# Kernel tuning notes

Hardware: AMD Instinct MI355X
Metric: run time of the kernel (lower is better)

Reference implementation:

```python
import jax, jax.numpy as jnp
import numpy as np

H, MEL, ATT, TXT = 1024, 80, 640, 640   # n_hidden, n_mel, n_attn_channels, n_text+n_speaker
T, TTXT = 600, 128


def setup_inputs() -> dict:
    key = jax.random.key(0)
    ks = jax.random.split(key, 20)
    def w(k, shape, s=0.02):
        return (jax.random.normal(k, shape) * s).astype(jnp.float32)
    return {
        "residual": jax.random.normal(ks[0], (T, 1, MEL), jnp.float32),
        "text": jax.random.normal(ks[1], (TTXT, 1, TXT), jnp.float32),
        # attention_lstm: LSTM(MEL -> H), 1 layer
        "Wih_a": w(ks[2], (4 * H, MEL)), "Whh_a": w(ks[3], (4 * H, H)),
        "bih_a": jnp.zeros(4 * H, jnp.float32), "bhh_a": jnp.zeros(4 * H, jnp.float32),
        # Attention: query/key/value projections + scoring vector v
        "Wq": w(ks[4], (ATT, H)), "Wk": w(ks[5], (ATT, TXT)), "Wv": w(ks[6], (ATT, TXT)),
        "v_w": w(ks[7], (ATT,)),
        # decoder lstm: LSTM(H+ATT -> H), 2 layers
        "Wih0": w(ks[8], (4 * H, H + ATT)), "Whh0": w(ks[9], (4 * H, H)),
        "bih0": jnp.zeros(4 * H, jnp.float32), "bhh0": jnp.zeros(4 * H, jnp.float32),
        "Wih1": w(ks[10], (4 * H, H)), "Whh1": w(ks[11], (4 * H, H)),
        "bih1": jnp.zeros(4 * H, jnp.float32), "bhh1": jnp.zeros(4 * H, jnp.float32),
        # DenseLayer: two tanh(Linear(H,H))
        "D0w": w(ks[12], (H, H)), "D0b": jnp.zeros(H, jnp.float32),
        "D1w": w(ks[13], (H, H)), "D1b": jnp.zeros(H, jnp.float32),
        # Conv1d(H, 2*MEL, kernel=1) == Linear
        "conv_w": w(ks[14], (2 * MEL, H)), "conv_b": jnp.zeros(2 * MEL, jnp.float32),
        # gate layer: Linear(H+ATT, 1)
        "gate_w": w(ks[15], (H + ATT,)), "gate_b": jnp.zeros((), jnp.float32),
    }


def lstm_cell(x, h, c, Wih, Whh, bih, bhh):
    # PyTorch gate order: i, f, g, o
    g = Wih @ x + bih + Whh @ h + bhh
    i, f, gg, o = jnp.split(g, 4)
    c2 = jax.nn.sigmoid(f) * c + jax.nn.sigmoid(i) * jnp.tanh(gg)
    return jax.nn.sigmoid(o) * jnp.tanh(c2), c2


def ar_back_step(residual, text, Wih_a, Whh_a, bih_a, bhh_a, Wq, Wk, Wv, v_w,
                 Wih0, Whh0, bih0, bhh0, Wih1, Whh1, bih1, bhh1,
                 D0w, D0b, D1w, D1b, conv_w, conv_b, gate_w, gate_b):
    res = residual[::-1, 0, :]            # AR_Back_Step flips time; batch=1 squeezed
    txt = text[:, 0, :]                   # [TTXT, TXT]
    K = txt @ Wk.T                        # [TTXT, ATT]  (keys constant over steps)
    V = txt @ Wv.T                        # [TTXT, ATT]
    z = jnp.zeros(H, jnp.float32)
    carry0 = (jnp.zeros(MEL, jnp.float32), z, z, z, z, z, z)

    def step(carry, r_t):
        out_prev, h, c, h0, c0, h1, c1 = carry
        # attention LSTM on previous output
        h, c = lstm_cell(out_prev, h, c, Wih_a, Whh_a, bih_a, bhh_a)
        # additive (Bahdanau-style) attention: v . tanh(q + K)
        q = Wq @ h                                   # [ATT]
        scores = jnp.tanh(q[None, :] + K) @ v_w      # [TTXT]
        attn = jax.nn.softmax(scores)
        ctx = attn @ V                               # [ATT]
        dec_in = jnp.concatenate([h, ctx])           # [H+ATT]
        # 2-layer decoder LSTM
        h0, c0 = lstm_cell(dec_in, h0, c0, Wih0, Whh0, bih0, bhh0)
        h1, c1 = lstm_cell(h0, h1, c1, Wih1, Whh1, bih1, bhh1)
        # DenseLayer (tanh MLP) then 1x1 conv
        d = jnp.tanh(D1w @ jnp.tanh(D0w @ h1 + D0b) + D1b)
        dec_out = conv_w @ d + conv_b                # [2*MEL]
        log_s, b = dec_out[:MEL], dec_out[MEL:]
        out = (r_t - b) / jnp.exp(log_s)             # affine coupling inverse
        gate = jax.nn.sigmoid(gate_w @ dec_in + gate_b)
        return (out, h, c, h0, c0, h1, c1), (out, gate)

    _, (outs, gates) = jax.lax.scan(step, carry0, res)
    total = outs[::-1][:, None, :]                   # flip back, restore batch dim
    return total, gates


def reference(residual, text, Wih_a, Whh_a, bih_a, bhh_a, Wq, Wk, Wv, v_w,
              Wih0, Whh0, bih0, bhh0, Wih1, Whh1, bih1, bhh1,
              D0w, D0b, D1w, D1b, conv_w, conv_b, gate_w, gate_b):
    return ar_back_step(residual, text, Wih_a, Whh_a, bih_a, bhh_a, Wq, Wk, Wv, v_w,
                        Wih0, Whh0, bih0, bhh0, Wih1, Whh1, bih1, bhh1,
                        D0w, D0b, D1w, D1b, conv_w, conv_b, gate_w, gate_b)
```

## Files before the change

kernel.cpp:

```cpp
#include <hip/hip_runtime.h>

#define NBLK 256
#define NTHR 1024

constexpr int H = 1024, MEL = 80, ATT = 640, TXTD = 640, T = 600, TTXT = 128;
constexpr int G4 = 4096, DIN = H + ATT;
constexpr int QPB = 5;

constexpr int WS_K     = 0;
constexpr int WS_V     = WS_K + TTXT * ATT;
constexpr int WS_HV    = WS_V + TTXT * ATT;
constexpr int WS_H0V   = WS_HV + H;
constexpr int WS_H1V   = WS_H0V + H;
constexpr int WS_SVP   = WS_H1V + H;
constexpr int WS_GH    = WS_SVP + 8 * TTXT;
constexpr int WS_DEC   = (WS_GH + 1 + 15) & ~15;
constexpr int WS_A0    = (WS_DEC + 2 * MEL + 15) & ~15;
constexpr int WS_END   = WS_A0 + H;
constexpr int WS_BAR   = (WS_END + 63) & ~63;

constexpr int SM_W0  = 0;
constexpr int SM_H   = SM_W0 + 16 * DIN;
constexpr int SM_H0  = SM_H + H;
constexpr int SM_H1  = SM_H0 + H;
constexpr int SM_A0  = SM_H1 + H;
constexpr int SM_KT  = SM_A0 + H;
constexpr int SM_VWL = SM_KT + QPB * TTXT;
constexpr int SM_QL  = SM_VWL + 8;
constexpr int SM_OUT = SM_QL + 8;
constexpr int SM_DEC = SM_OUT + MEL;
constexpr int SM_RED = SM_DEC + 2 * MEL;
constexpr int SM_D   = SM_RED + 16;
constexpr int SM_M   = SM_D + 4 + 8;
constexpr int SM_MG  = SM_M + 16 * TTXT;
constexpr int SM_SV  = SM_MG + TTXT;
constexpr int SM_CNT = SM_SV + TTXT;
constexpr size_t SM_BYTES = ((size_t)SM_CNT * 4 + 255) & ~(size_t)255;

#define KEEP4(v) \
  asm volatile("" : "+v"((v).x), "+v"((v).y), "+v"((v).z), "+v"((v).w))

struct Params {
  const float *residual, *text, *Wih_a, *Whh_a, *bih_a, *bhh_a,
      *Wq, *Wk, *Wv, *v_w, *Wih0, *Whh0, *bih0, *bhh0,
      *Wih1, *Whh1, *bih1, *bhh1, *D0w, *D0b, *D1w, *D1b,
      *conv_w, *conv_b, *gate_w, *gate_b;
  float* out;
  float* ws;
};

__device__ __forceinline__ float sigm(float x) { return 1.0f / (1.0f + __expf(-x)); }
__device__ __forceinline__ float ftanh(float x) {
  x = fminf(15.f, fmaxf(-15.f, x));
  float e = __expf(2.f * x);
  return (e - 1.f) / (e + 1.f);
}

__device__ __forceinline__ float aload(const float* p) {
  return __hip_atomic_load(p, __ATOMIC_RELAXED, __HIP_MEMORY_SCOPE_AGENT);
}
__device__ __forceinline__ void astore(float* p, float v) {
  __hip_atomic_store(p, v, __ATOMIC_RELAXED, __HIP_MEMORY_SCOPE_AGENT);
}

__device__ __forceinline__ void g_arrive(unsigned* bar) {
  asm volatile("s_waitcnt vmcnt(0)" ::: "memory");
  __syncthreads();
  if (threadIdx.x == 0) {
    unsigned* leaf = bar + (blockIdx.x & 15) * 32;
    unsigned o = __hip_atomic_fetch_add(leaf, 1u, __ATOMIC_RELAXED,
                                        __HIP_MEMORY_SCOPE_AGENT);
    if ((o & 15) == 15)
      __hip_atomic_fetch_add(bar + 544, 1u, __ATOMIC_RELAXED,
                             __HIP_MEMORY_SCOPE_AGENT);
  }
}
__device__ __forceinline__ void g_wait(unsigned* bar, unsigned target) {
  if (threadIdx.x == 0) {
    while (__hip_atomic_load(bar + 544, __ATOMIC_RELAXED,
                             __HIP_MEMORY_SCOPE_AGENT) < target)
      __builtin_amdgcn_s_sleep(1);
  }
  __syncthreads();
}

__device__ __forceinline__ float red64(float s) {
#pragma unroll
  for (int off = 32; off; off >>= 1) s += __shfl_xor(s, off, 64);
  return s;
}

__device__ __forceinline__ float dot16pin(float4 w0, float4 w1, float4 w2,
                                          float4 w3, const float* x, int lane) {
  const float4* x4 = (const float4*)x;
  float4 b0 = x4[lane], b1 = x4[lane + 64], b2 = x4[lane + 128],
         b3 = x4[lane + 192];
  float s0 = w0.x * b0.x, s1 = w1.x * b1.x;
  s0 = fmaf(w0.y, b0.y, s0); s1 = fmaf(w1.y, b1.y, s1);
  s0 = fmaf(w0.z, b0.z, s0); s1 = fmaf(w1.z, b1.z, s1);
  s0 = fmaf(w0.w, b0.w, s0); s1 = fmaf(w1.w, b1.w, s1);
  s0 = fmaf(w2.x, b2.x, s0); s1 = fmaf(w3.x, b3.x, s1);
  s0 = fmaf(w2.y, b2.y, s0); s1 = fmaf(w3.y, b3.y, s1);
  s0 = fmaf(w2.z, b2.z, s0); s1 = fmaf(w3.z, b3.z, s1);
  s0 = fmaf(w2.w, b2.w, s0); s1 = fmaf(w3.w, b3.w, s1);
  return s0 + s1;
}

__device__ __forceinline__ float dot16load(const float* w, const float* x,
                                           int lane) {
  const float4* w4 = (const float4*)w;
  const float4* x4 = (const float4*)x;
  float4 a0 = w4[lane], a1 = w4[lane + 64], a2 = w4[lane + 128],
         a3 = w4[lane + 192];
  float4 b0 = x4[lane], b1 = x4[lane + 64], b2 = x4[lane + 128],
         b3 = x4[lane + 192];
  float s0 = a0.x * b0.x, s1 = a1.x * b1.x;
  s0 = fmaf(a0.y, b0.y, s0); s1 = fmaf(a1.y, b1.y, s1);
  s0 = fmaf(a0.z, b0.z, s0); s1 = fmaf(a1.z, b1.z, s1);
  s0 = fmaf(a0.w, b0.w, s0); s1 = fmaf(a1.w, b1.w, s1);
  s0 = fmaf(a2.x, b2.x, s0); s1 = fmaf(a3.x, b3.x, s1);
  s0 = fmaf(a2.y, b2.y, s0); s1 = fmaf(a3.y, b3.y, s1);
  s0 = fmaf(a2.z, b2.z, s0); s1 = fmaf(a3.z, b3.z, s1);
  s0 = fmaf(a2.w, b2.w, s0); s1 = fmaf(a3.w, b3.w, s1);
  return s0 + s1;
}

__device__ __forceinline__ float wave_dot(const float* __restrict__ w,
                                          const float* __restrict__ x,
                                          int n4, int lane) {
  float s = 0.f;
  const float4* w4 = (const float4*)w;
  const float4* x4 = (const float4*)x;
  for (int i = lane; i < n4; i += 64) {
    float4 a = w4[i];
    float4 b = x4[i];
    s = fmaf(a.x, b.x, s);
    s = fmaf(a.y, b.y, s);
    s = fmaf(a.z, b.z, s);
    s = fmaf(a.w, b.w, s);
  }
  return red64(s);
}

__global__ void __launch_bounds__(NTHR, 4) ar_kernel(Params p) {
  const int b = blockIdx.x;
  const int tid = threadIdx.x;
  const int wave = tid >> 6;
  const int lane = tid & 63;
  const int sg = wave >> 2;
  const int wg = wave & 3;
  const int gw = b * 16 + wave;

  float* ws = p.ws;
  float* Kw = ws + WS_K;
  float* Vw = ws + WS_V;
  float* hv = ws + WS_HV;
  float* h0v = ws + WS_H0V;
  float* h1v = ws + WS_H1V;
  float* svp = ws + WS_SVP;
  float* ghp = ws + WS_GH;
  float* dec = ws + WS_DEC;
  float* a0g = ws + WS_A0;
  unsigned* bar = (unsigned*)(ws + WS_BAR);

  extern __shared__ __align__(16) float smem[];
  float* s_w0 = smem + SM_W0;
  float* s_h = smem + SM_H;
  float* s_h0 = smem + SM_H0;
  float* s_h1 = smem + SM_H1;
  float* s_a0 = smem + SM_A0;
  float* s_kt = smem + SM_KT;
  float* s_vwl = smem + SM_VWL;
  float* s_ql = smem + SM_QL;
  float* s_out = smem + SM_OUT;
  float* s_dec = smem + SM_DEC;
  float* s_red = smem + SM_RED;
  float* s_d = smem + SM_D;
  float* s_m = smem + SM_M;
  float* s_mg = smem + SM_MG;
  float* s_sv = smem + SM_SV;

  const int e = 4 * b + sg;
  const int grow = e + wg * H;

  const float4* WA = (const float4*)(p.Whh_a + (size_t)grow * H);
  float4 wa0 = WA[lane], wa1 = WA[lane + 64], wa2 = WA[lane + 128],
         wa3 = WA[lane + 192];
  KEEP4(wa0); KEEP4(wa1); KEEP4(wa2); KEEP4(wa3);
  const float4* W0 = (const float4*)(p.Whh0 + (size_t)grow * H);
  float4 w00 = W0[lane], w01 = W0[lane + 64], w02 = W0[lane + 128],
         w03 = W0[lane + 192];
  KEEP4(w00); KEEP4(w01); KEEP4(w02); KEEP4(w03);
  const float4* W1 = (const float4*)(p.Whh1 + (size_t)grow * H);
  float4 w10 = W1[lane], w11 = W1[lane + 64], w12 = W1[lane + 128],
         w13 = W1[lane + 192];
  KEEP4(w10); KEEP4(w11); KEEP4(w12); KEEP4(w13);
  const float4* WI = (const float4*)(p.Wih1 + (size_t)grow * H);
  float4 wi0 = WI[lane], wi1 = WI[lane + 64], wi2 = WI[lane + 128],
         wi3 = WI[lane + 192];
  KEEP4(wi0); KEEP4(wi1); KEEP4(wi2); KEEP4(wi3);
  float4 wma = make_float4(0.f, 0.f, 0.f, 0.f);
  if (lane < MEL / 4)
    wma = ((const float4*)(p.Wih_a + (size_t)grow * MEL))[lane];
  KEEP4(wma);
  float4 wf = ((const float4*)(p.D0w + (size_t)e * H))[wg * 64 + lane];
  KEEP4(wf);
  float4 wgd = ((const float4*)(p.D1w + (size_t)e * H))[wg * 64 + lane];
  KEEP4(wgd);
  float4 wcv = make_float4(0.f, 0.f, 0.f, 0.f);
  if (tid < 2 * MEL) wcv = ((const float4*)(p.conv_w + (size_t)tid * H))[b];
  KEEP4(wcv);
  const float ba = p.bih_a[grow] + p.bhh_a[grow];
  const float b0s = p.bih0[grow] + p.bhh0[grow];
  const float b1s = p.bih1[grow] + p.bhh1[grow];

  {
    const float4* src = (const float4*)(p.Wih0 + (size_t)grow * DIN);
    float4* dst = (float4*)(s_w0 + wave * DIN);
    for (int i = lane; i < DIN / 4; i += 64) dst[i] = src[i];
  }
  if (b < TTXT && tid < QPB) s_vwl[tid] = p.v_w[QPB * b + tid];
  s_h[tid] = 0.f;
  s_h0[tid] = 0.f;
  s_h1[tid] = 0.f;

  float c_reg = 0.f, c0_reg = 0.f, c1_reg = 0.f;
  float u0_reg = 0.f, u1_reg = 0.f, w0h_reg = 0.f;

  unsigned bk = 0;

  for (int idx = gw; idx < 2 * TTXT * ATT; idx += NBLK * 16) {
    int isV = idx >= TTXT * ATT;
    int rem = isV ? idx - TTXT * ATT : idx;
    int j = rem / ATT;
    int a = rem - j * ATT;
    const float* wrow = (isV ? p.Wv : p.Wk) + a * TXTD;
    float s = wave_dot(wrow, p.text + j * TXTD, TXTD / 4, lane);
    if (lane == 0) astore(&(isV ? Vw : Kw)[j * ATT + a], s);
  }
  if (b == 0)
    for (int i = tid; i < 8 * TTXT; i += NTHR) astore(&svp[i], 0.f);
  g_arrive(bar); ++bk; g_wait(bar, 16 * bk);
  if (b < TTXT) {
    for (int i = tid; i < QPB * TTXT; i += NTHR) {
      int a = i >> 7, d = i & (TTXT - 1);
      s_kt[i] = aload(&Kw[d * ATT + QPB * b + a]);
    }
  }
  {
    const float4* wrow = (const float4*)(s_w0 + wave * DIN + H);
    for (int j = 0; j < TTXT; ++j) {
      const float4* v4 = (const float4*)(Vw + j * ATT);
      float s = 0.f;
      for (int i = lane; i < ATT / 4; i += 64) {
        float4 a = wrow[i], x = v4[i];
        s = fmaf(a.x, x.x, s);
        s = fmaf(a.y, x.y, s);
        s = fmaf(a.z, x.z, s);
        s = fmaf(a.w, x.w, s);
      }
      s = red64(s);
      if (lane == 0) s_m[wave * TTXT + j] = s;
    }
  }
  if (b == 0) {
    for (int j = wave; j < TTXT; j += 16) {
      float s = wave_dot(p.gate_w + H, Vw + j * ATT, ATT / 4, lane);
      if (lane == 0) s_mg[j] = s;
    }
  }
  __syncthreads();

  for (int t = 0; t < T; ++t) {
    if (tid < 2 * MEL) s_dec[tid] = aload(dec + tid);
    __syncthreads();
    if (tid < MEL) {
      float o = 0.f;
      if (t != 0) {
        float ls = s_dec[tid] + p.conv_b[tid];
        float bb = s_dec[MEL + tid] + p.conv_b[MEL + tid];
        float r = p.residual[(T - t) * MEL + tid];
        o = (r - bb) * __expf(-ls);
        if (b == 0) p.out[(T - t) * MEL + tid] = o;
      }
      s_out[tid] = o;
    }
    __syncthreads();
    {
      float pa = dot16pin(wa0, wa1, wa2, wa3, s_h, lane);
      if (lane < MEL / 4) {
        float4 bm = ((const float4*)s_out)[lane];
        pa = fmaf(wma.x, bm.x, pa);
        pa = fmaf(wma.y, bm.y, pa);
        pa = fmaf(wma.z, bm.z, pa);
        pa = fmaf(wma.w, bm.w, pa);
      }
      pa = red64(pa);
      if (lane == 0) s_red[wave] = pa + ba;
      __syncthreads();
      if (tid < 4) {
        int ee = 4 * b + tid;
        float gi = s_red[tid * 4 + 0], gf = s_red[tid * 4 + 1];
        float gg = s_red[tid * 4 + 2], go = s_red[tid * 4 + 3];
        float c2 = sigm(gf) * c_reg + sigm(gi) * ftanh(gg);
        c_reg = c2;
        astore(&hv[ee], sigm(go) * ftanh(c2));
      }
    }
    g_arrive(bar); ++bk;
    g_wait(bar, 16 * bk);

    s_h[tid] = aload(hv + tid);
    __syncthreads();
    if (b < TTXT && wave < QPB) {
      float q = red64(
          dot16load(p.Wq + (size_t)(QPB * b + wave) * H, s_h, lane));
      if (lane == 0) s_ql[wave] = q;
    }
    if (b == NBLK - 1) {
      if (wave == 15) {
        float q = wave_dot(p.gate_w, s_h, H / 4, lane);
        if (lane == 0) astore(&ghp[0], q);
      }
      for (int i = tid; i < 2 * MEL; i += NTHR) astore(&dec[i], 0.f);
    }
    __syncthreads();
    if (b < TTXT && tid < TTXT) {
      float partial = 0.f;
#pragma unroll
      for (int a = 0; a < QPB; ++a)
        partial = fmaf(s_vwl[a], ftanh(s_ql[a] + s_kt[a * TTXT + tid]),
                       partial);
      atomicAdd(&svp[(b & 7) * TTXT + tid], partial);
    }
    g_arrive(bar); ++bk;
    w0h_reg = red64(dot16load(s_w0 + wave * DIN, s_h, lane));
    g_wait(bar, 16 * bk);

    {
      if (tid < TTXT) {
        float s8 = aload(&svp[tid]);
#pragma unroll
        for (int g = 1; g < 8; ++g) s8 += aload(&svp[g * TTXT + tid]);
        s_sv[tid] = s8;
      }
      __syncthreads();
      float pa_ = __expf(s_sv[lane] - 16.f);
      float pb_ = __expf(s_sv[lane + 64] - 16.f);
      float den_ = red64(pa_ + pb_);
      float w0c = red64(fmaf(pa_, s_m[wave * TTXT + lane],
                             pb_ * s_m[wave * TTXT + lane + 64]));
      if (lane == 0) s_red[wave] = w0c / den_ + w0h_reg + u0_reg + b0s;
      __syncthreads();
      if (tid < 4) {
        int ee = 4 * b + tid;
        float gi = s_red[tid * 4 + 0], gf = s_red[tid * 4 + 1];
        float gg = s_red[tid * 4 + 2], go = s_red[tid * 4 + 3];
        float c2 = sigm(gf) * c0_reg + sigm(gi) * ftanh(gg);
        c0_reg = c2;
        astore(&h0v[ee], sigm(go) * ftanh(c2));
      }
    }
    g_arrive(bar); ++bk;
    if (b == 0 && wave == 15) {
      float pa_ = __expf(s_sv[lane] - 16.f);
      float pb_ = __expf(s_sv[lane + 64] - 16.f);
      float den_ = red64(pa_ + pb_);
      float gc = red64(fmaf(pa_, s_mg[lane], pb_ * s_mg[lane + 64]));
      if (lane == 0) {
        float gh = aload(&ghp[0]);
        p.out[T * MEL + t] = sigm(gh + gc / den_ + p.gate_b[0]);
      }
    }
    g_wait(bar, 16 * bk);

    s_h0[tid] = aload(h0v + tid);
    __syncthreads();
    {
      float pe = dot16pin(wi0, wi1, wi2, wi3, s_h0, lane);
      pe = red64(pe);
      if (lane == 0) s_red[wave] = pe + u1_reg + b1s;
      __syncthreads();
      if (tid < 4) {
        int ee = 4 * b + tid;
        float gi = s_red[tid * 4 + 0], gf = s_red[tid * 4 + 1];
        float gg = s_red[tid * 4 + 2], go = s_red[tid * 4 + 3];
        float c2 = sigm(gf) * c1_reg + sigm(gi) * ftanh(gg);
        c1_reg = c2;
        astore(&h1v[ee], sigm(go) * ftanh(c2));
      }
    }
    if (b == NBLK - 1 && tid < 8 * TTXT)
      astore(&svp[tid], 0.f);
    g_arrive(bar); ++bk;
    u0_reg = red64(dot16pin(w00, w01, w02, w03, s_h0, lane));
    g_wait(bar, 16 * bk);

    s_h1[tid] = aload(h1v + tid);
    __syncthreads();
    {
      float4 x = ((const float4*)s_h1)[wg * 64 + lane];
      float s = wf.x * x.x;
      s = fmaf(wf.y, x.y, s); s = fmaf(wf.z, x.z, s); s = fmaf(wf.w, x.w, s);
      s = red64(s);
      if (lane == 0) s_red[wave] = s;
      __syncthreads();
      if (tid < 4) {
        int r2 = 4 * b + tid;
        float tot = s_red[tid * 4] + s_red[tid * 4 + 1] + s_red[tid * 4 + 2] +
                    s_red[tid * 4 + 3];
        astore(&a0g[r2], ftanh(tot + p.D0b[r2]));
      }
    }
    g_arrive(bar); ++bk;
    u1_reg = red64(dot16pin(w10, w11, w12, w13, s_h1, lane));
    g_wait(bar, 16 * bk);

    s_a0[tid] = aload(a0g + tid);
    __syncthreads();
    {
      float4 x = ((const float4*)s_a0)[wg * 64 + lane];
      float s = wgd.x * x.x;
      s = fmaf(wgd.y, x.y, s); s = fmaf(wgd.z, x.z, s); s = fmaf(wgd.w, x.w, s);
      s = red64(s);
      if (lane == 0) s_red[wave] = s;
      __syncthreads();
      if (tid < 4) {
        int r2 = 4 * b + tid;
        float tot = s_red[tid * 4] + s_red[tid * 4 + 1] + s_red[tid * 4 + 2] +
                    s_red[tid * 4 + 3];
        s_d[tid] = ftanh(tot + p.D1b[r2]);
      }
      __syncthreads();
      if (tid < 2 * MEL) {
        float acc = wcv.x * s_d[0];
        acc = fmaf(wcv.y, s_d[1], acc);
        acc = fmaf(wcv.z, s_d[2], acc);
        acc = fmaf(wcv.w, s_d[3], acc);
        atomicAdd(&dec[tid], acc);
      }
    }
    g_arrive(bar); ++bk;
    g_wait(bar, 16 * bk);
  }

  if (b == 0 && tid < MEL) {
    float ls = aload(&dec[tid]) + p.conv_b[tid];
    float bb = aload(&dec[MEL + tid]) + p.conv_b[MEL + tid];
    float r = p.residual[tid];
    p.out[tid] = (r - bb) * __expf(-ls);
  }
}

extern "C" void kernel_launch(void* const* d_in, const int* in_sizes, int n_in,
                              void* d_out, int out_size, void* d_ws, size_t ws_size,
                              hipStream_t stream) {
  Params hp;
  hp.residual = (const float*)d_in[0];
  hp.text = (const float*)d_in[1];
  hp.Wih_a = (const float*)d_in[2];
  hp.Whh_a = (const float*)d_in[3];
  hp.bih_a = (const float*)d_in[4];
  hp.bhh_a = (const float*)d_in[5];
  hp.Wq = (const float*)d_in[6];
  hp.Wk = (const float*)d_in[7];
  hp.Wv = (const float*)d_in[8];
  hp.v_w = (const float*)d_in[9];
  hp.Wih0 = (const float*)d_in[10];
  hp.Whh0 = (const float*)d_in[11];
  hp.bih0 = (const float*)d_in[12];
  hp.bhh0 = (const float*)d_in[13];
  hp.Wih1 = (const float*)d_in[14];
  hp.Whh1 = (const float*)d_in[15];
  hp.bih1 = (const float*)d_in[16];
  hp.bhh1 = (const float*)d_in[17];
  hp.D0w = (const float*)d_in[18];
  hp.D0b = (const float*)d_in[19];
  hp.D1w = (const float*)d_in[20];
  hp.D1b = (const float*)d_in[21];
  hp.conv_w = (const float*)d_in[22];
  hp.conv_b = (const float*)d_in[23];
  hp.gate_w = (const float*)d_in[24];
  hp.gate_b = (const float*)d_in[25];
  hp.out = (float*)d_out;
  hp.ws = (float*)d_ws;

  hipMemsetAsync((char*)d_ws + (size_t)WS_BAR * sizeof(float), 0, 4096, stream);

  void* args[] = {&hp};
  hipLaunchCooperativeKernel((void*)ar_kernel, dim3(NBLK), dim3(NTHR), args,
                             (uint32_t)SM_BYTES, stream);
}
```

Before: 23.85 ms.

## Overlap attention-LSTM hidden dot with barrier wait and preload Wq rows

The attention LSTM's Whh·h dot product is moved from the start of the next step into the window between grid-barrier arrive and wait at the end of the current step, so the barrier latency hides that compute. The Wq and gate weight rows are loaded into registers before the hidden-state fetch so their global-memory latency overlaps the barrier read and __syncthreads. Launch bounds are relaxed from 4 to 2 blocks per SM, which gives more registers to hold the extra float4 values at the cost of lower occupancy hints.

Result: slower. 25.39 ms (+6.5%).

```diff
diff --git a/kernel.cpp b/kernel.cpp
--- a/kernel.cpp
+++ b/kernel.cpp
@@ -142,7 +142,7 @@
   return red64(s);
 }
 
-__global__ void __launch_bounds__(NTHR, 4) ar_kernel(Params p) {
+__global__ void __launch_bounds__(NTHR, 2) ar_kernel(Params p) {
   const int b = blockIdx.x;
   const int tid = threadIdx.x;
   const int wave = tid >> 6;
@@ -225,7 +225,7 @@
   s_h1[tid] = 0.f;
 
   float c_reg = 0.f, c0_reg = 0.f, c1_reg = 0.f;
-  float u0_reg = 0.f, u1_reg = 0.f, w0h_reg = 0.f;
+  float u0_reg = 0.f, u1_reg = 0.f, w0h_reg = 0.f, pa_reg = 0.f;
 
   unsigned bk = 0;
 
@@ -287,16 +287,16 @@
     }
     __syncthreads();
     {
-      float pa = dot16pin(wa0, wa1, wa2, wa3, s_h, lane);
+      float wred = 0.f;
       if (lane < MEL / 4) {
         float4 bm = ((const float4*)s_out)[lane];
-        pa = fmaf(wma.x, bm.x, pa);
-        pa = fmaf(wma.y, bm.y, pa);
-        pa = fmaf(wma.z, bm.z, pa);
-        pa = fmaf(wma.w, bm.w, pa);
-      }
-      pa = red64(pa);
-      if (lane == 0) s_red[wave] = pa + ba;
+        wred = wma.x * bm.x;
+        wred = fmaf(wma.y, bm.y, wred);
+        wred = fmaf(wma.z, bm.z, wred);
+        wred = fmaf(wma.w, bm.w, wred);
+      }
+      wred = red64(wred);
+      if (lane == 0) s_red[wave] = pa_reg + wred + ba;
       __syncthreads();
       if (tid < 4) {
         int ee = 4 * b + tid;
@@ -310,28 +310,41 @@
     g_arrive(bar); ++bk;
     g_wait(bar, 16 * bk);
 
-    s_h[tid] = aload(hv + tid);
-    __syncthreads();
-    if (b < TTXT && wave < QPB) {
-      float q = red64(
-          dot16load(p.Wq + (size_t)(QPB * b + wave) * H, s_h, lane));
-      if (lane == 0) s_ql[wave] = q;
-    }
-    if (b == NBLK - 1) {
-      if (wave == 15) {
-        float q = wave_dot(p.gate_w, s_h, H / 4, lane);
+    {
+      float4 qw0, qw1, qw2, qw3;
+      const bool qown = (b < TTXT) && (wave < QPB);
+      const bool gown = (b == NBLK - 1) && (wave == 15);
+      if (qown) {
+        const float4* W4 =
+            (const float4*)(p.Wq + (size_t)(QPB * b + wave) * H);
+        qw0 = W4[lane]; qw1 = W4[lane + 64];
+        qw2 = W4[lane + 128]; qw3 = W4[lane + 192];
+      } else if (gown) {
+        const float4* W4 = (const float4*)p.gate_w;
+        qw0 = W4[lane]; qw1 = W4[lane + 64];
+        qw2 = W4[lane + 128]; qw3 = W4[lane + 192];
+      }
+      s_h[tid] = aload(hv + tid);
+      __syncthreads();
+      if (qown) {
+        float q = red64(dot16pin(qw0, qw1, qw2, qw3, s_h, lane));
+        if (lane == 0) s_ql[wave] = q;
+      } else if (gown) {
+        float q = red64(dot16pin(qw0, qw1, qw2, qw3, s_h, lane));
         if (lane == 0) astore(&ghp[0], q);
       }
-      for (int i = tid; i < 2 * MEL; i += NTHR) astore(&dec[i], 0.f);
-    }
-    __syncthreads();
-    if (b < TTXT && tid < TTXT) {
-      float partial = 0.f;
+      if (b == NBLK - 1) {
+        for (int i = tid; i < 2 * MEL; i += NTHR) astore(&dec[i], 0.f);
+      }
+      __syncthreads();
+      if (b < TTXT && tid < TTXT) {
+        float partial = 0.f;
 #pragma unroll
-      for (int a = 0; a < QPB; ++a)
-        partial = fmaf(s_vwl[a], ftanh(s_ql[a] + s_kt[a * TTXT + tid]),
-                       partial);
-      atomicAdd(&svp[(b & 7) * TTXT + tid], partial);
+        for (int a = 0; a < QPB; ++a)
+          partial = fmaf(s_vwl[a], ftanh(s_ql[a] + s_kt[a * TTXT + tid]),
+                         partial);
+        atomicAdd(&svp[(b & 7) * TTXT + tid], partial);
+      }
     }
     g_arrive(bar); ++bk;
     w0h_reg = red64(dot16load(s_w0 + wave * DIN, s_h, lane));
@@ -441,6 +454,7 @@
       }
     }
     g_arrive(bar); ++bk;
+    pa_reg = red64(dot16pin(wa0, wa1, wa2, wa3, s_h, lane));
     g_wait(bar, 16 * bk);
   }
 
```
